# Kernel optimization log

Hardware: AMD Instinct MI355X
Metric: run time of the kernel (lower is better)

## Reference

```python
import jax, jax.numpy as jnp
import numpy as np

N_NODES = 100000
N_EDGES = 3200000
N_GRAPHS = 64
NEG_SLOPE = 0.2


def mish(x):
    return x * jnp.tanh(jax.nn.softplus(x))


def gat_layer(x, src, dst, W, b, a_src, a_dst, heads, out_ch, n_nodes):
    # h: [N, H, C]
    h = (x @ W).reshape(n_nodes, heads, out_ch)
    alpha_s = jnp.sum(h * a_src[None], axis=-1)  # [N, H]
    alpha_d = jnp.sum(h * a_dst[None], axis=-1)  # [N, H]
    e = jax.nn.leaky_relu(alpha_s[src] + alpha_d[dst], NEG_SLOPE)  # [E, H]
    # scatter-softmax over incoming edges of each destination node
    emax = jax.ops.segment_max(e, dst, num_segments=n_nodes)  # [N, H]
    ee = jnp.exp(e - emax[dst])
    den = jax.ops.segment_sum(ee, dst, num_segments=n_nodes)
    alpha = ee / (den[dst] + 1e-16)  # [E, H]
    msg = h[src] * alpha[..., None]  # [E, H, C]
    out = jax.ops.segment_sum(msg, dst, num_segments=n_nodes)
    return out.reshape(n_nodes, heads * out_ch) + b


def setup_inputs() -> dict:
    key = jax.random.key(0)
    ks = jax.random.split(key, 10)
    x = jax.random.normal(ks[0], (N_NODES, 128), dtype=jnp.float32)
    edge_index = jax.random.randint(ks[1], (2, N_EDGES), 0, N_NODES, dtype=jnp.int64)
    batch = jnp.sort(jax.random.randint(ks[2], (N_NODES,), 0, N_GRAPHS, dtype=jnp.int64))
    s1 = 1.0 / np.sqrt(128.0)
    s2 = 1.0 / np.sqrt(16.0)
    return {
        "x": x,
        "edge_index": edge_index,
        "batch": batch,
        "W1": jax.random.normal(ks[3], (128, 16), dtype=jnp.float32) * s1,
        "b1": jnp.zeros((16,), dtype=jnp.float32),
        "a_src1": jax.random.normal(ks[4], (4, 4), dtype=jnp.float32) * 0.5,
        "a_dst1": jax.random.normal(ks[5], (4, 4), dtype=jnp.float32) * 0.5,
        "W2": jax.random.normal(ks[6], (16, 32), dtype=jnp.float32) * s2,
        "b2": jnp.zeros((32,), dtype=jnp.float32),
        "a_src2": jax.random.normal(ks[7], (1, 32), dtype=jnp.float32) * 0.5,
        "a_dst2": jax.random.normal(ks[8], (1, 32), dtype=jnp.float32) * 0.5,
    }


def reference(x, edge_index, batch, W1, b1, a_src1, a_dst1, W2, b2, a_src2, a_dst2):
    n = x.shape[0]
    # PyG GATConv default add_self_loops=True
    loop = jnp.arange(n, dtype=edge_index.dtype)
    src = jnp.concatenate([edge_index[0], loop])
    dst = jnp.concatenate([edge_index[1], loop])
    h = mish(gat_layer(x, src, dst, W1, b1, a_src1, a_dst1, heads=4, out_ch=4, n_nodes=n))
    h = mish(gat_layer(h, src, dst, W2, b2, a_src2, a_dst2, heads=1, out_ch=32, n_nodes=n))
    # global_mean_pool
    sums = jax.ops.segment_sum(h, batch, num_segments=N_GRAPHS)
    cnts = jax.ops.segment_sum(jnp.ones((n,), h.dtype), batch, num_segments=N_GRAPHS)
    return sums / jnp.maximum(cnts, 1.0)[:, None]
```

## Files before the change

kernel.cpp:

```cpp
#include <hip/hip_runtime.h>
#include <hip/hip_fp16.h>
#include <math.h>

#define NEG_SLOPE 0.2f
#define SB 256
#define NBMAX 1024

typedef _Float16 half2v __attribute__((ext_vector_type(2)));

__device__ __forceinline__ float mishf(float x) {
    if (x > 15.f) return x;
    float ex = __expf(x);
    float y = 1.f + ex;
    float y2 = y * y;
    return x * (y2 - 1.f) / (y2 + 1.f);
}

__device__ __forceinline__ float lw(float e) {
    return __expf(fmaxf(e, NEG_SLOPE * e));
}

__device__ __forceinline__ float hdot2(half2v a, half2v b) {
#if __has_builtin(__builtin_amdgcn_fdot2)
    return __builtin_amdgcn_fdot2(a, b, 0.f, false);
#else
    return (float)a.x * (float)b.x + (float)a.y * (float)b.y;
#endif
}

__global__ void gemm1_kernel(const float* __restrict__ x, const float* __restrict__ W1,
                             const float* __restrict__ a_dst,
                             _Float16* __restrict__ hpre1h, float* __restrict__ addst, int N) {
    __shared__ float Wl[128 * 16];
    __shared__ float xs[16 * 132];
    int tid = threadIdx.x;
    for (int i = tid; i < 2048; i += 256) Wl[i] = W1[i];
    int nodebase = blockIdx.x * 16;
    const float4* x4 = (const float4*)(x + (size_t)nodebase * 128);
    for (int i = tid; i < 512; i += 256) {
        float4 v = x4[i];
        int e = i * 4;
        int nl = e >> 7, k = e & 127;
        float* dp = &xs[nl * 132 + k];
        dp[0] = v.x; dp[1] = v.y; dp[2] = v.z; dp[3] = v.w;
    }
    __syncthreads();
    int nl = tid >> 4, ch = tid & 15;
    const float* xr = &xs[nl * 132];
    float acc = 0.f;
    #pragma unroll 8
    for (int k = 0; k < 128; k++) acc += xr[k] * Wl[k * 16 + ch];
    int node = nodebase + nl;
    if (node < N) {
        hpre1h[node * 16 + ch] = (_Float16)acc;
        float pd = acc * a_dst[ch];
        pd += __shfl_xor(pd, 1); pd += __shfl_xor(pd, 2);
        if ((ch & 3) == 0) addst[node * 4 + (ch >> 2)] = pd;
    }
}

__global__ void prep2_kernel(const float* __restrict__ W2, const float* __restrict__ as2,
                             const float* __restrict__ ad2,
                             float* __restrict__ vs, float* __restrict__ vd) {
    int t = threadIdx.x;
    if (t < 16) {
        float s = 0.f, d = 0.f;
        #pragma unroll
        for (int c = 0; c < 32; c++) {
            float w = W2[t * 32 + c];
            s += w * as2[c];
            d += w * ad2[c];
        }
        vs[t] = s; vd[t] = d;
    }
}

__global__ __launch_bounds__(1024) void histE_kernel(
        const int* __restrict__ dst, int E, int Etot, int CH, int NB,
        int* __restrict__ hist) {
    __shared__ int cnt[NBMAX];
    int tid = threadIdx.x, blk = blockIdx.x;
    for (int b = tid; b < NB; b += 1024) cnt[b] = 0;
    __syncthreads();
    int iend = min((blk + 1) * CH, Etot);
    for (int i = blk * CH + tid; i < iend; i += 1024) {
        int d = (i < E) ? dst[i] : (i - E);
        atomicAdd(&cnt[d >> 7], 1);
    }
    __syncthreads();
    for (int b = tid; b < NB; b += 1024) hist[b * SB + blk] = cnt[b];
}

__global__ void scanA_kernel(const int* __restrict__ in, int T, int* __restrict__ incl, int* __restrict__ bsum) {
    __shared__ int s[512];
    int t = threadIdx.x;
    int i = blockIdx.x * 512 + t;
    s[t] = (i < T) ? in[i] : 0;
    __syncthreads();
    for (int off = 1; off < 512; off <<= 1) {
        int v = (t >= off) ? s[t - off] : 0;
        __syncthreads();
        s[t] += v;
        __syncthreads();
    }
    if (i < T) incl[i] = s[t];
    if (t == 511) bsum[blockIdx.x] = s[511];
}

__global__ void scanB_kernel(int* __restrict__ bsum, int nb) {
    __shared__ int s[512];
    int t = threadIdx.x;
    s[t] = (t < nb) ? bsum[t] : 0;
    __syncthreads();
    for (int off = 1; off < 512; off <<= 1) {
        int v = (t >= off) ? s[t - off] : 0;
        __syncthreads();
        s[t] += v;
        __syncthreads();
    }
    if (t < nb) bsum[t] = s[t];
}

__global__ void scanC_kernel(const int* __restrict__ in, const int* __restrict__ incl,
                             const int* __restrict__ bsum, int T, int* __restrict__ sbase) {
    int i = blockIdx.x * 512 + threadIdx.x;
    if (i >= T) return;
    int off = (blockIdx.x > 0) ? bsum[blockIdx.x - 1] : 0;
    sbase[i] = incl[i] - in[i] + off;
}

__global__ __launch_bounds__(1024) void scatE_kernel(
        const int* __restrict__ src, const int* __restrict__ dst,
        int E, int Etot, int CH, int NB,
        const int* __restrict__ sbase, int* __restrict__ pairs) {
    __shared__ int lcnt[NBMAX];
    __shared__ int lbase[NBMAX];
    int tid = threadIdx.x, blk = blockIdx.x;
    for (int b = tid; b < NB; b += 1024) { lcnt[b] = 0; lbase[b] = sbase[b * SB + blk]; }
    __syncthreads();
    int iend = min((blk + 1) * CH, Etot);
    for (int i = blk * CH + tid; i < iend; i += 1024) {
        int s, d;
        if (i < E) { s = src[i]; d = dst[i]; } else { s = d = i - E; }
        int b = d >> 7, dl = d & 127;
        int r = atomicAdd(&lcnt[b], 1);
        pairs[lbase[b] + r] = s | (dl << 17);
    }
}

__global__ __launch_bounds__(1024) void localcsr_kernel(
        const int* __restrict__ pairs, const int* __restrict__ sbase,
        int Etot, int NB, int N,
        int* __restrict__ ssorted, int* __restrict__ row_start) {
    __shared__ int deg[128];
    __shared__ int s[128];
    __shared__ int cur[128];
    int tid = threadIdx.x, b = blockIdx.x;
    int nb0 = b << 7;
    int cnt_nodes = min(128, N - nb0);
    int start = sbase[b * SB];
    int end = (b + 1 < NB) ? sbase[(b + 1) * SB] : Etot;
    if (tid < 128) deg[tid] = 0;
    __syncthreads();
    for (int j = start + tid; j < end; j += 1024)
        atomicAdd(&deg[(pairs[j] >> 17) & 127], 1);
    __syncthreads();
    if (tid < 128) s[tid] = deg[tid];
    __syncthreads();
    for (int o = 1; o < 128; o <<= 1) {
        int v = 0;
        if (tid < 128 && tid >= o) v = s[tid - o];
        __syncthreads();
        if (tid < 128) s[tid] += v;
        __syncthreads();
    }
    if (tid < 128) {
        int ex = start + s[tid] - deg[tid];
        cur[tid] = ex;
        if (tid < cnt_nodes) row_start[nb0 + tid] = ex;
    }
    if (b == NB - 1 && tid == 0) row_start[N] = end;
    __syncthreads();
    for (int j = start + tid; j < end; j += 1024) {
        int p = pairs[j];
        int pos = atomicAdd(&cur[(p >> 17) & 127], 1);
        ssorted[pos] = p & 0x1FFFF;
    }
}

__global__ void agg1_kernel(const int* __restrict__ row_start, const int* __restrict__ ssorted,
                            const float* __restrict__ a_src1, const float* __restrict__ addst,
                            const _Float16* __restrict__ hpre1h,
                            const float* __restrict__ b1,
                            const float* __restrict__ vs, const float* __restrict__ vd,
                            _Float16* __restrict__ hpost1h,
                            float* __restrict__ as2n, float* __restrict__ ad2n, int N) {
    int wave = threadIdx.x >> 6;
    int lane = threadIdx.x & 63;
    int node = blockIdx.x * 4 + wave;
    if (node >= N) return;
    int start = row_start[node], end = row_start[node + 1];
    int er = lane >> 3, hc = lane & 7, head = hc >> 1;
    int c0 = hc * 2;
    half2v wsh;
    wsh.x = (_Float16)a_src1[c0];
    wsh.y = (_Float16)a_src1[c0 + 1];
    float adh = addst[node * 4 + head];
    const _Float16* hb = hpre1h + c0;
    float den = 0.f, a0 = 0.f, a1 = 0.f;
    int last = end - 1;
    int jb = start;
    for (; jb + 16 <= end; jb += 16) {
        int j0 = jb + er, j1 = j0 + 8;
        int s0 = __builtin_nontemporal_load(ssorted + j0);
        int s1 = __builtin_nontemporal_load(ssorted + j1);
        half2v h0 = *(const half2v*)(hb + s0 * 16);
        half2v h1 = *(const half2v*)(hb + s1 * 16);
        float p0 = hdot2(h0, wsh);
        float p1 = hdot2(h1, wsh);
        float w0 = lw(p0 + __shfl_xor(p0, 1) + adh);
        float w1 = lw(p1 + __shfl_xor(p1, 1) + adh);
        den += w0 + w1;
        a0 += (float)h0.x * w0 + (float)h1.x * w1;
        a1 += (float)h0.y * w0 + (float)h1.y * w1;
    }
    if (jb < end) {
        int j0 = jb + er, j1 = j0 + 8;
        int k0 = (j0 <= last) ? j0 : last;
        int k1 = (j1 <= last) ? j1 : last;
        int s0 = __builtin_nontemporal_load(ssorted + k0);
        int s1 = __builtin_nontemporal_load(ssorted + k1);
        half2v h0 = *(const half2v*)(hb + s0 * 16);
        half2v h1 = *(const half2v*)(hb + s1 * 16);
        float p0 = hdot2(h0, wsh);
        float p1 = hdot2(h1, wsh);
        float e0 = p0 + __shfl_xor(p0, 1) + adh;
        float e1 = p1 + __shfl_xor(p1, 1) + adh;
        float w0 = (j0 <= last) ? lw(e0) : 0.f;
        float w1 = (j1 <= last) ? lw(e1) : 0.f;
        den += w0 + w1;
        a0 += (float)h0.x * w0 + (float)h1.x * w1;
        a1 += (float)h0.y * w0 + (float)h1.y * w1;
    }
    a0 += __shfl_xor(a0, 8);  a1 += __shfl_xor(a1, 8);  den += __shfl_xor(den, 8);
    a0 += __shfl_xor(a0, 16); a1 += __shfl_xor(a1, 16); den += __shfl_xor(den, 16);
    a0 += __shfl_xor(a0, 32); a1 += __shfl_xor(a1, 32); den += __shfl_xor(den, 32);
    if (er == 0) {
        float inv = 1.f / (den + 1e-16f);
        float o0 = mishf(a0 * inv + b1[c0]);
        float o1 = mishf(a1 * inv + b1[c0 + 1]);
        half2v oh;
        oh.x = (_Float16)o0; oh.y = (_Float16)o1;
        *(half2v*)(hpost1h + node * 16 + c0) = oh;
        float ps = o0 * vs[c0] + o1 * vs[c0 + 1];
        float pd = o0 * vd[c0] + o1 * vd[c0 + 1];
        ps += __shfl_xor(ps, 1); pd += __shfl_xor(pd, 1);
        ps += __shfl_xor(ps, 2); pd += __shfl_xor(pd, 2);
        ps += __shfl_xor(ps, 4); pd += __shfl_xor(pd, 4);
        if (hc == 0) { as2n[node] = ps; ad2n[node] = pd; }
    }
}

__global__ void agg2_kernel(const int* __restrict__ row_start, const int* __restrict__ ssorted,
                            const float* __restrict__ as2n, const float* __restrict__ ad2n,
                            const _Float16* __restrict__ hpost1h,
                            float* __restrict__ agg16, float* __restrict__ denv, int N) {
    int wave = threadIdx.x >> 6;
    int lane = threadIdx.x & 63;
    int node = blockIdx.x * 4 + wave;
    if (node >= N) return;
    int start = row_start[node], end = row_start[node + 1];
    int er = lane >> 3, hc = lane & 7;
    int c0 = hc * 2;
    float adh = ad2n[node];
    const _Float16* hb = hpost1h + c0;
    float den = 0.f, a0 = 0.f, a1 = 0.f;
    int last = end - 1;
    int jb = start;
    for (; jb + 16 <= end; jb += 16) {
        int j0 = jb + er, j1 = j0 + 8;
        int s0 = __builtin_nontemporal_load(ssorted + j0);
        int s1 = __builtin_nontemporal_load(ssorted + j1);
        float e0 = as2n[s0] + adh;
        float e1 = as2n[s1] + adh;
        half2v h0 = *(const half2v*)(hb + s0 * 16);
        half2v h1 = *(const half2v*)(hb + s1 * 16);
        float w0 = lw(e0);
        float w1 = lw(e1);
        den += w0 + w1;
        a0 += (float)h0.x * w0 + (float)h1.x * w1;
        a1 += (float)h0.y * w0 + (float)h1.y * w1;
    }
    if (jb < end) {
        int j0 = jb + er, j1 = j0 + 8;
        int k0 = (j0 <= last) ? j0 : last;
        int k1 = (j1 <= last) ? j1 : last;
        int s0 = __builtin_nontemporal_load(ssorted + k0);
        int s1 = __builtin_nontemporal_load(ssorted + k1);
        float e0 = as2n[s0] + adh;
        float e1 = as2n[s1] + adh;
        half2v h0 = *(const half2v*)(hb + s0 * 16);
        half2v h1 = *(const half2v*)(hb + s1 * 16);
        float w0 = (j0 <= last) ? lw(e0) : 0.f;
        float w1 = (j1 <= last) ? lw(e1) : 0.f;
        den += w0 + w1;
        a0 += (float)h0.x * w0 + (float)h1.x * w1;
        a1 += (float)h0.y * w0 + (float)h1.y * w1;
    }
    a0 += __shfl_xor(a0, 8);  a1 += __shfl_xor(a1, 8);  den += __shfl_xor(den, 8);
    a0 += __shfl_xor(a0, 16); a1 += __shfl_xor(a1, 16); den += __shfl_xor(den, 16);
    a0 += __shfl_xor(a0, 32); a1 += __shfl_xor(a1, 32); den += __shfl_xor(den, 32);
    if (er == 0) {
        float2 o; o.x = a0; o.y = a1;
        *(float2*)(agg16 + node * 16 + c0) = o;
        if (hc == 0) denv[node] = den;
    }
}

__global__ void post2_kernel(const float* __restrict__ agg16, const float* __restrict__ denv,
                             const float* __restrict__ W2, const float* __restrict__ b2,
                             float* __restrict__ hpost2, int N) {
    __shared__ float Wl[16 * 32];
    __shared__ float hs[8 * 20];
    __shared__ float dsh[8];
    int tid = threadIdx.x;
    for (int i = tid; i < 512; i += 256) Wl[i] = W2[i];
    int nodebase = blockIdx.x * 8;
    const float4* h4 = (const float4*)(agg16 + (size_t)nodebase * 16);
    if (tid < 32) {
        float4 v = h4[tid];
        int e = tid * 4;
        int nl = e >> 4, k = e & 15;
        float* dp = &hs[nl * 20 + k];
        dp[0] = v.x; dp[1] = v.y; dp[2] = v.z; dp[3] = v.w;
    }
    if (tid < 8) {
        int n = nodebase + tid;
        dsh[tid] = denv[(n < N) ? n : (N - 1)];
    }
    __syncthreads();
    int nl = tid >> 5, ch = tid & 31;
    const float* hr = &hs[nl * 20];
    float acc = 0.f;
    #pragma unroll
    for (int k = 0; k < 16; k++) acc += hr[k] * Wl[k * 32 + ch];
    int node = nodebase + nl;
    if (node < N) {
        float val = acc / (dsh[nl] + 1e-16f) + b2[ch];
        hpost2[(size_t)node * 32 + ch] = mishf(val);
    }
}

__global__ void pool_kernel(const float* __restrict__ hpost2, const int* __restrict__ batch,
                            int N, float* __restrict__ pool, float* __restrict__ cnt) {
    int tid = threadIdx.x;
    int r = tid >> 5, ch = tid & 31;
    int base = blockIdx.x * 512;
    int cur = -1;
    float sum = 0.f, c = 0.f;
    for (int it = 0; it < 64; it++) {
        int n = base + it * 8 + r;
        if (n >= N) break;
        int g = batch[n];
        if (g != cur) {
            if (cur >= 0) {
                atomicAdd(&pool[cur * 32 + ch], sum);
                if (ch == 0) atomicAdd(&cnt[cur], c);
            }
            cur = g; sum = 0.f; c = 0.f;
        }
        sum += hpost2[(size_t)n * 32 + ch];
        c += 1.f;
    }
    if (cur >= 0) {
        atomicAdd(&pool[cur * 32 + ch], sum);
        if (ch == 0) atomicAdd(&cnt[cur], c);
    }
}

__global__ void fin_kernel(const float* __restrict__ pool, const float* __restrict__ cnt,
                           float* __restrict__ out, int NG) {
    int i = blockIdx.x * blockDim.x + threadIdx.x;
    if (i >= NG * 32) return;
    out[i] = pool[i] / fmaxf(cnt[i >> 5], 1.0f);
}

extern "C" void kernel_launch(void* const* d_in, const int* in_sizes, int n_in,
                              void* d_out, int out_size, void* d_ws, size_t ws_size,
                              hipStream_t stream) {
    const float* x   = (const float*)d_in[0];
    const int* eidx  = (const int*)d_in[1];
    const int* batch = (const int*)d_in[2];
    const float* W1  = (const float*)d_in[3];
    const float* b1  = (const float*)d_in[4];
    const float* as1 = (const float*)d_in[5];
    const float* ad1 = (const float*)d_in[6];
    const float* W2  = (const float*)d_in[7];
    const float* b2  = (const float*)d_in[8];
    const float* as2 = (const float*)d_in[9];
    const float* ad2 = (const float*)d_in[10];
    float* out = (float*)d_out;

    int N = in_sizes[0] / 128;
    int E = in_sizes[1] / 2;
    int Etot = E + N;
    int NG = out_size / 32;
    const int* esrc = eidx;
    const int* edst = eidx + E;

    int NB = (N + 127) >> 7;
    int CH = (Etot + SB - 1) / SB;
    int T  = NB * SB;
    int TB = (T + 511) / 512;

    char* p = (char*)d_ws;
    auto alloc = [&](size_t nbytes) {
        p = (char*)(((uintptr_t)p + 15) & ~(uintptr_t)15);
        void* r = (void*)p; p += nbytes; return r;
    };
    int* hist      = (int*)alloc((size_t)T * 4);
    int* incl      = (int*)alloc((size_t)T * 4);
    int* bsum      = (int*)alloc(512 * 4);
    int* sbase     = (int*)alloc((size_t)T * 4);
    int* pairs     = (int*)alloc((size_t)Etot * 4);
    int* ssorted   = (int*)alloc((size_t)Etot * 4);
    int* row_start = (int*)alloc((size_t)(N + 1) * 4);
    _Float16* hpre1h  = (_Float16*)alloc((size_t)N * 16 * 2);
    _Float16* hpost1h = (_Float16*)alloc((size_t)N * 16 * 2);
    float* addst1  = (float*)alloc((size_t)N * 4 * 4);
    float* as2n    = (float*)alloc((size_t)N * 4);
    float* ad2n    = (float*)alloc((size_t)N * 4);
    float* agg16   = (float*)alloc((size_t)N * 16 * 4);
    float* denv    = (float*)alloc((size_t)N * 4);
    float* hpost2  = (float*)alloc((size_t)N * 32 * 4);
    float* vs      = (float*)alloc(16 * 4);
    float* vd      = (float*)alloc(16 * 4);
    float* pool    = (float*)alloc((size_t)NG * 32 * 4);
    float* cnt     = (float*)alloc((size_t)NG * 4);

    hipMemsetAsync(pool, 0, (size_t)NG * 32 * 4, stream);
    hipMemsetAsync(cnt, 0, (size_t)NG * 4, stream);

    gemm1_kernel<<<(N + 15) / 16, 256, 0, stream>>>(x, W1, ad1, hpre1h, addst1, N);
    prep2_kernel<<<1, 64, 0, stream>>>(W2, as2, ad2, vs, vd);
    histE_kernel<<<SB, 1024, 0, stream>>>(edst, E, Etot, CH, NB, hist);
    scanA_kernel<<<TB, 512, 0, stream>>>(hist, T, incl, bsum);
    scanB_kernel<<<1, 512, 0, stream>>>(bsum, TB);
    scanC_kernel<<<TB, 512, 0, stream>>>(hist, incl, bsum, T, sbase);
    scatE_kernel<<<SB, 1024, 0, stream>>>(esrc, edst, E, Etot, CH, NB, sbase, pairs);
    localcsr_kernel<<<NB, 1024, 0, stream>>>(pairs, sbase, Etot, NB, N, ssorted, row_start);
    agg1_kernel<<<(N + 3) / 4, 256, 0, stream>>>(row_start, ssorted, as1, addst1, hpre1h,
                                                 b1, vs, vd, hpost1h, as2n, ad2n, N);
    agg2_kernel<<<(N + 3) / 4, 256, 0, stream>>>(row_start, ssorted, as2n, ad2n, hpost1h,
                                                 agg16, denv, N);
    post2_kernel<<<(N + 7) / 8, 256, 0, stream>>>(agg16, denv, W2, b2, hpost2, N);
    pool_kernel<<<(N + 511) / 512, 256, 0, stream>>>(hpost2, batch, N, pool, cnt);
    fin_kernel<<<(NG * 32 + 255) / 256, 256, 0, stream>>>(pool, cnt, out, NG);
}
```

Baseline: 380.0 us.

## Replace three-pass scan with atomic bucket cursors and fuse post2 with pooling

The per-bucket histogram now also accumulates bucket totals atomically. A single setup kernel scans those totals and also holds the W2 projection prep. The scatter kernel claims per-block offsets with atomics on cursors, which removes the three scan kernels and the large sbase array. Buffer zeroing moves into gemm1 in place of memsets, and post2 is fused with mean pooling so the N×32 intermediate is never written. The cost is atomic-ordered bucket layout (nondeterministic within a bucket) and more pool atomics per 8-node block.

```diff
diff --git a/kernel.cpp b/kernel.cpp
--- a/kernel.cpp
+++ b/kernel.cpp
@@ -30,10 +30,17 @@
 
 __global__ void gemm1_kernel(const float* __restrict__ x, const float* __restrict__ W1,
                              const float* __restrict__ a_dst,
-                             _Float16* __restrict__ hpre1h, float* __restrict__ addst, int N) {
+                             _Float16* __restrict__ hpre1h, float* __restrict__ addst,
+                             int* __restrict__ bucket_total, float* __restrict__ pool,
+                             float* __restrict__ cnt, int NB, int NG, int N) {
     __shared__ float Wl[128 * 16];
     __shared__ float xs[16 * 132];
     int tid = threadIdx.x;
+    if (blockIdx.x == 0) {
+        for (int i = tid; i < NB; i += 256) bucket_total[i] = 0;
+        for (int i = tid; i < NG * 32; i += 256) pool[i] = 0.f;
+        for (int i = tid; i < NG; i += 256) cnt[i] = 0.f;
+    }
     for (int i = tid; i < 2048; i += 256) Wl[i] = W1[i];
     int nodebase = blockIdx.x * 16;
     const float4* x4 = (const float4*)(x + (size_t)nodebase * 128);
@@ -59,25 +66,9 @@
     }
 }
 
-__global__ void prep2_kernel(const float* __restrict__ W2, const float* __restrict__ as2,
-                             const float* __restrict__ ad2,
-                             float* __restrict__ vs, float* __restrict__ vd) {
-    int t = threadIdx.x;
-    if (t < 16) {
-        float s = 0.f, d = 0.f;
-        #pragma unroll
-        for (int c = 0; c < 32; c++) {
-            float w = W2[t * 32 + c];
-            s += w * as2[c];
-            d += w * ad2[c];
-        }
-        vs[t] = s; vd[t] = d;
-    }
-}
-
-__global__ __launch_bounds__(1024) void histE_kernel(
+__global__ __launch_bounds__(1024) void histB_kernel(
         const int* __restrict__ dst, int E, int Etot, int CH, int NB,
-        int* __restrict__ hist) {
+        int* __restrict__ hist, int* __restrict__ bucket_total) {
     __shared__ int cnt[NBMAX];
     int tid = threadIdx.x, blk = blockIdx.x;
     for (int b = tid; b < NB; b += 1024) cnt[b] = 0;
@@ -88,55 +79,59 @@
         atomicAdd(&cnt[d >> 7], 1);
     }
     __syncthreads();
-    for (int b = tid; b < NB; b += 1024) hist[b * SB + blk] = cnt[b];
-}
-
-__global__ void scanA_kernel(const int* __restrict__ in, int T, int* __restrict__ incl, int* __restrict__ bsum) {
-    __shared__ int s[512];
+    for (int b = tid; b < NB; b += 1024) {
+        int c = cnt[b];
+        hist[b * SB + blk] = c;
+        if (c) atomicAdd(&bucket_total[b], c);
+    }
+}
+
+__global__ __launch_bounds__(1024) void setup_kernel(
+        const int* __restrict__ bucket_total, int NB,
+        int* __restrict__ bucket_base, int* __restrict__ cursor,
+        const float* __restrict__ W2, const float* __restrict__ as2,
+        const float* __restrict__ ad2, float* __restrict__ vs, float* __restrict__ vd) {
+    __shared__ int s[1024];
     int t = threadIdx.x;
-    int i = blockIdx.x * 512 + t;
-    s[t] = (i < T) ? in[i] : 0;
-    __syncthreads();
-    for (int off = 1; off < 512; off <<= 1) {
+    int own = (t < NB) ? bucket_total[t] : 0;
+    s[t] = own;
+    __syncthreads();
+    for (int off = 1; off < 1024; off <<= 1) {
         int v = (t >= off) ? s[t - off] : 0;
         __syncthreads();
         s[t] += v;
         __syncthreads();
     }
-    if (i < T) incl[i] = s[t];
-    if (t == 511) bsum[blockIdx.x] = s[511];
-}
-
-__global__ void scanB_kernel(int* __restrict__ bsum, int nb) {
-    __shared__ int s[512];
-    int t = threadIdx.x;
-    s[t] = (t < nb) ? bsum[t] : 0;
-    __syncthreads();
-    for (int off = 1; off < 512; off <<= 1) {
-        int v = (t >= off) ? s[t - off] : 0;
-        __syncthreads();
-        s[t] += v;
-        __syncthreads();
-    }
-    if (t < nb) bsum[t] = s[t];
-}
-
-__global__ void scanC_kernel(const int* __restrict__ in, const int* __restrict__ incl,
-                             const int* __restrict__ bsum, int T, int* __restrict__ sbase) {
-    int i = blockIdx.x * 512 + threadIdx.x;
-    if (i >= T) return;
-    int off = (blockIdx.x > 0) ? bsum[blockIdx.x - 1] : 0;
-    sbase[i] = incl[i] - in[i] + off;
-}
-
-__global__ __launch_bounds__(1024) void scatE_kernel(
+    if (t < NB) {
+        int ex = s[t] - own;
+        bucket_base[t] = ex;
+        cursor[t] = ex;
+    }
+    if (t < 16) {
+        float ps = 0.f, pd = 0.f;
+        #pragma unroll
+        for (int c = 0; c < 32; c++) {
+            float w = W2[t * 32 + c];
+            ps += w * as2[c];
+            pd += w * ad2[c];
+        }
+        vs[t] = ps; vd[t] = pd;
+    }
+}
+
+__global__ __launch_bounds__(1024) void scatE2_kernel(
         const int* __restrict__ src, const int* __restrict__ dst,
         int E, int Etot, int CH, int NB,
-        const int* __restrict__ sbase, int* __restrict__ pairs) {
+        const int* __restrict__ hist, int* __restrict__ cursor,
+        int* __restrict__ pairs) {
     __shared__ int lcnt[NBMAX];
     __shared__ int lbase[NBMAX];
     int tid = threadIdx.x, blk = blockIdx.x;
-    for (int b = tid; b < NB; b += 1024) { lcnt[b] = 0; lbase[b] = sbase[b * SB + blk]; }
+    for (int b = tid; b < NB; b += 1024) {
+        lcnt[b] = 0;
+        int h = hist[b * SB + blk];
+        lbase[b] = h ? atomicAdd(&cursor[b], h) : 0;
+    }
     __syncthreads();
     int iend = min((blk + 1) * CH, Etot);
     for (int i = blk * CH + tid; i < iend; i += 1024) {
@@ -149,8 +144,8 @@
 }
 
 __global__ __launch_bounds__(1024) void localcsr_kernel(
-        const int* __restrict__ pairs, const int* __restrict__ sbase,
-        int Etot, int NB, int N,
+        const int* __restrict__ pairs, const int* __restrict__ bucket_base,
+        const int* __restrict__ bucket_total, int NB, int N,
         int* __restrict__ ssorted, int* __restrict__ row_start) {
     __shared__ int deg[128];
     __shared__ int s[128];
@@ -158,8 +153,8 @@
     int tid = threadIdx.x, b = blockIdx.x;
     int nb0 = b << 7;
     int cnt_nodes = min(128, N - nb0);
-    int start = sbase[b * SB];
-    int end = (b + 1 < NB) ? sbase[(b + 1) * SB] : Etot;
+    int start = bucket_base[b];
+    int end = start + bucket_total[b];
     if (tid < 128) deg[tid] = 0;
     __syncthreads();
     for (int j = start + tid; j < end; j += 1024)
@@ -317,12 +312,15 @@
     }
 }
 
-__global__ void post2_kernel(const float* __restrict__ agg16, const float* __restrict__ denv,
-                             const float* __restrict__ W2, const float* __restrict__ b2,
-                             float* __restrict__ hpost2, int N) {
+__global__ void post2pool_kernel(const float* __restrict__ agg16, const float* __restrict__ denv,
+                                 const float* __restrict__ W2, const float* __restrict__ b2,
+                                 const int* __restrict__ batch,
+                                 float* __restrict__ pool, float* __restrict__ cnt, int N) {
     __shared__ float Wl[16 * 32];
     __shared__ float hs[8 * 20];
     __shared__ float dsh[8];
+    __shared__ int gsh[8];
+    __shared__ float arr[8 * 33];
     int tid = threadIdx.x;
     for (int i = tid; i < 512; i += 256) Wl[i] = W2[i];
     int nodebase = blockIdx.x * 8;
@@ -337,6 +335,7 @@
     if (tid < 8) {
         int n = nodebase + tid;
         dsh[tid] = denv[(n < N) ? n : (N - 1)];
+        gsh[tid] = (n < N) ? batch[n] : -1;
     }
     __syncthreads();
     int nl = tid >> 5, ch = tid & 31;
@@ -345,36 +344,22 @@
     #pragma unroll
     for (int k = 0; k < 16; k++) acc += hr[k] * Wl[k * 32 + ch];
     int node = nodebase + nl;
-    if (node < N) {
-        float val = acc / (dsh[nl] + 1e-16f) + b2[ch];
-        hpost2[(size_t)node * 32 + ch] = mishf(val);
-    }
-}
-
-__global__ void pool_kernel(const float* __restrict__ hpost2, const int* __restrict__ batch,
-                            int N, float* __restrict__ pool, float* __restrict__ cnt) {
-    int tid = threadIdx.x;
-    int r = tid >> 5, ch = tid & 31;
-    int base = blockIdx.x * 512;
-    int cur = -1;
-    float sum = 0.f, c = 0.f;
-    for (int it = 0; it < 64; it++) {
-        int n = base + it * 8 + r;
-        if (n >= N) break;
-        int g = batch[n];
-        if (g != cur) {
-            if (cur >= 0) {
-                atomicAdd(&pool[cur * 32 + ch], sum);
-                if (ch == 0) atomicAdd(&cnt[cur], c);
-            }
-            cur = g; sum = 0.f; c = 0.f;
+    float val = 0.f;
+    if (node < N) val = mishf(acc / (dsh[nl] + 1e-16f) + b2[ch]);
+    arr[nl * 33 + ch] = val;
+    __syncthreads();
+    if (tid < 32) {
+        int i = 0;
+        while (i < 8) {
+            int g = gsh[i];
+            if (g < 0) break;
+            float s = 0.f;
+            int j = i;
+            while (j < 8 && gsh[j] == g) { s += arr[j * 33 + tid]; j++; }
+            atomicAdd(&pool[g * 32 + tid], s);
+            if (tid == 0) atomicAdd(&cnt[g], (float)(j - i));
+            i = j;
         }
-        sum += hpost2[(size_t)n * 32 + ch];
-        c += 1.f;
-    }
-    if (cur >= 0) {
-        atomicAdd(&pool[cur * 32 + ch], sum);
-        if (ch == 0) atomicAdd(&cnt[cur], c);
     }
 }
 
@@ -411,20 +396,19 @@
     int NB = (N + 127) >> 7;
     int CH = (Etot + SB - 1) / SB;
     int T  = NB * SB;
-    int TB = (T + 511) / 512;
 
     char* p = (char*)d_ws;
     auto alloc = [&](size_t nbytes) {
         p = (char*)(((uintptr_t)p + 15) & ~(uintptr_t)15);
         void* r = (void*)p; p += nbytes; return r;
     };
-    int* hist      = (int*)alloc((size_t)T * 4);
-    int* incl      = (int*)alloc((size_t)T * 4);
-    int* bsum      = (int*)alloc(512 * 4);
-    int* sbase     = (int*)alloc((size_t)T * 4);
-    int* pairs     = (int*)alloc((size_t)Etot * 4);
-    int* ssorted   = (int*)alloc((size_t)Etot * 4);
-    int* row_start = (int*)alloc((size_t)(N + 1) * 4);
+    int* hist         = (int*)alloc((size_t)T * 4);
+    int* pairs        = (int*)alloc((size_t)Etot * 4);
+    int* ssorted      = (int*)alloc((size_t)Etot * 4);
+    int* row_start    = (int*)alloc((size_t)(N + 1) * 4);
+    int* bucket_total = (int*)alloc((size_t)NB * 4);
+    int* bucket_base  = (int*)alloc((size_t)NB * 4);
+    int* cursor       = (int*)alloc((size_t)NB * 4);
     _Float16* hpre1h  = (_Float16*)alloc((size_t)N * 16 * 2);
     _Float16* hpost1h = (_Float16*)alloc((size_t)N * 16 * 2);
     float* addst1  = (float*)alloc((size_t)N * 4 * 4);
@@ -432,28 +416,24 @@
     float* ad2n    = (float*)alloc((size_t)N * 4);
     float* agg16   = (float*)alloc((size_t)N * 16 * 4);
     float* denv    = (float*)alloc((size_t)N * 4);
-    float* hpost2  = (float*)alloc((size_t)N * 32 * 4);
     float* vs      = (float*)alloc(16 * 4);
     float* vd      = (float*)alloc(16 * 4);
     float* pool    = (float*)alloc((size_t)NG * 32 * 4);
     float* cnt     = (float*)alloc((size_t)NG * 4);
 
-    hipMemsetAsync(pool, 0, (size_t)NG * 32 * 4, stream);
-    hipMemsetAsync(cnt, 0, (size_t)NG * 4, stream);
-
-    gemm1_kernel<<<(N + 15) / 16, 256, 0, stream>>>(x, W1, ad1, hpre1h, addst1, N);
-    prep2_kernel<<<1, 64, 0, stream>>>(W2, as2, ad2, vs, vd);
-    histE_kernel<<<SB, 1024, 0, stream>>>(edst, E, Etot, CH, NB, hist);
-    scanA_kernel<<<TB, 512, 0, stream>>>(hist, T, incl, bsum);
-    scanB_kernel<<<1, 512, 0, stream>>>(bsum, TB);
-    scanC_kernel<<<TB, 512, 0, stream>>>(hist, incl, bsum, T, sbase);
-    scatE_kernel<<<SB, 1024, 0, stream>>>(esrc, edst, E, Etot, CH, NB, sbase, pairs);
-    localcsr_kernel<<<NB, 1024, 0, stream>>>(pairs, sbase, Etot, NB, N, ssorted, row_start);
+    gemm1_kernel<<<(N + 15) / 16, 256, 0, stream>>>(x, W1, ad1, hpre1h, addst1,
+                                                    bucket_total, pool, cnt, NB, NG, N);
+    histB_kernel<<<SB, 1024, 0, stream>>>(edst, E, Etot, CH, NB, hist, bucket_total);
+    setup_kernel<<<1, 1024, 0, stream>>>(bucket_total, NB, bucket_base, cursor,
+                                         W2, as2, ad2, vs, vd);
+    scatE2_kernel<<<SB, 1024, 0, stream>>>(esrc, edst, E, Etot, CH, NB, hist, cursor, pairs);
+    localcsr_kernel<<<NB, 1024, 0, stream>>>(pairs, bucket_base, bucket_total, NB, N,
+                                             ssorted, row_start);
     agg1_kernel<<<(N + 3) / 4, 256, 0, stream>>>(row_start, ssorted, as1, addst1, hpre1h,
                                                  b1, vs, vd, hpost1h, as2n, ad2n, N);
     agg2_kernel<<<(N + 3) / 4, 256, 0, stream>>>(row_start, ssorted, as2n, ad2n, hpost1h,
                                                  agg16, denv, N);
-    post2_kernel<<<(N + 7) / 8, 256, 0, stream>>>(agg16, denv, W2, b2, hpost2, N);
-    pool_kernel<<<(N + 511) / 512, 256, 0, stream>>>(hpost2, batch, N, pool, cnt);
+    post2pool_kernel<<<(N + 7) / 8, 256, 0, stream>>>(agg16, denv, W2, b2, batch,
+                                                      pool, cnt, N);
     fin_kernel<<<(NG * 32 + 255) / 256, 256, 0, stream>>>(pool, cnt, out, NG);
 }
```

Measured after the change: 419.8 us. +10.5%, slower.
